# Optimization experiments

Hardware: AMD Instinct MI355X
Metric: run time of the kernel (lower is better)

## Reference

```python
import jax, jax.numpy as jnp
import numpy as np

D_MODEL = 1024
D_STATE = 16
D_CONV = 4
EXPAND = 2
D_INNER = EXPAND * D_MODEL          # 2048
DT_RANK = D_MODEL // 16             # 64 (ceil(d_model/16))
BATCH = 4
SEQ = 2048


def setup_inputs() -> dict:
    key = jax.random.key(0)
    ks = jax.random.split(key, 9)
    s = lambda k, shape, sc: jax.random.normal(k, shape, jnp.float32) * sc
    x = s(ks[0], (BATCH, SEQ, D_MODEL), 1.0)
    W_in = s(ks[1], (2 * D_INNER, D_MODEL), D_MODEL ** -0.5)       # in_proj (no bias)
    conv_w = s(ks[2], (D_INNER, D_CONV), D_CONV ** -0.5)           # depthwise causal conv1d
    conv_b = s(ks[3], (D_INNER,), 0.02)
    W_xproj = s(ks[4], (DT_RANK + 2 * D_STATE, D_INNER), D_INNER ** -0.5)  # x_proj (no bias)
    W_dt = s(ks[5], (D_INNER, DT_RANK), DT_RANK ** -0.5)           # dt_proj weight
    b_dt = jax.random.uniform(ks[6], (D_INNER,), jnp.float32, -4.0, -1.0)  # dt_proj bias (small dt init)
    # S4D-real init: A_log = log([1..d_state]) per channel
    A_log = jnp.log(jnp.tile(jnp.arange(1, D_STATE + 1, dtype=jnp.float32), (D_INNER, 1)))
    D_skip = jnp.ones((D_INNER,), jnp.float32)
    W_out = s(ks[7], (D_MODEL, D_INNER), D_INNER ** -0.5)          # out_proj (no bias)
    return dict(x=x, W_in=W_in, conv_w=conv_w, conv_b=conv_b, W_xproj=W_xproj,
                W_dt=W_dt, b_dt=b_dt, A_log=A_log, D_skip=D_skip, W_out=W_out)


def reference(x, W_in, conv_w, conv_b, W_xproj, W_dt, b_dt, A_log, D_skip, W_out):
    silu = jax.nn.silu
    # in_proj -> split into x stream and gate z
    xz = jnp.einsum('bld,ed->ble', x, W_in)              # (B, L, 2*d_inner)
    xi, z = jnp.split(xz, 2, axis=-1)
    # causal depthwise conv1d (pad left d_conv-1), small fixed K loop
    K = conv_w.shape[1]
    L = xi.shape[1]
    xpad = jnp.pad(xi, ((0, 0), (K - 1, 0), (0, 0)))
    xc = sum(xpad[:, k:k + L, :] * conv_w[:, k] for k in range(K))
    u = silu(xc + conv_b)                                # (B, L, d_inner)
    # x_proj -> dt, B, C
    dbl = jnp.einsum('blc,ec->ble', u, W_xproj)          # (B, L, dt_rank + 2*d_state)
    dt = jax.nn.softplus(jnp.einsum('blr,cr->blc', dbl[..., :DT_RANK], W_dt) + b_dt)  # (B,L,d_inner)
    Bs = dbl[..., DT_RANK:DT_RANK + D_STATE]             # (B, L, d_state)
    Cs = dbl[..., DT_RANK + D_STATE:]                    # (B, L, d_state)
    A = -jnp.exp(A_log)                                  # (d_inner, d_state)

    # selective scan: h_t = exp(dt_t * A) * h_{t-1} + dt_t * B_t * u_t ; y_t = <h_t, C_t>
    def step(h, inp):
        dt_t, B_t, C_t, u_t = inp                        # (B,d_inner),(B,ds),(B,ds),(B,d_inner)
        dA = jnp.exp(dt_t[:, :, None] * A)               # (B, d_inner, d_state)
        h = h * dA + (dt_t * u_t)[:, :, None] * B_t[:, None, :]
        y = jnp.einsum('bcs,bs->bc', h, C_t)
        return h, y

    h0 = jnp.zeros((x.shape[0], D_INNER, D_STATE), x.dtype)
    xs = (jnp.swapaxes(dt, 0, 1), jnp.swapaxes(Bs, 0, 1),
          jnp.swapaxes(Cs, 0, 1), jnp.swapaxes(u, 0, 1))
    _, ys = jax.lax.scan(step, h0, xs)                   # ys: (L, B, d_inner)
    y = jnp.swapaxes(ys, 0, 1) + u * D_skip              # skip connection D*u
    y = y * silu(z)                                      # gate
    return jnp.einsum('blc,dc->bld', y, W_out)           # out_proj -> (B, L, d_model)
```

## Files before the change

### kernel.cpp

```cpp
#include <hip/hip_runtime.h>

#define AS1 __attribute__((address_space(1)))
#define AS3 __attribute__((address_space(3)))

typedef unsigned short ushort_t;
typedef __attribute__((ext_vector_type(8))) short short8;
typedef __attribute__((ext_vector_type(4))) float floatx4;

__device__ __forceinline__ float bf2f(ushort_t h) {
    return __uint_as_float(((unsigned int)h) << 16);
}
__device__ __forceinline__ ushort_t f2bf(float f) {
    unsigned int u = __float_as_uint(f);
    u += 0x7fffu + ((u >> 16) & 1u);
    return (ushort_t)(u >> 16);
}

__global__ __launch_bounds__(256) void cast_all(
    const float* __restrict__ s0, ushort_t* __restrict__ d0,
    const float* __restrict__ s1, ushort_t* __restrict__ d1,
    const float* __restrict__ s2, ushort_t* __restrict__ d2,
    const float* __restrict__ s3, ushort_t* __restrict__ d3,
    const float* __restrict__ s4, ushort_t* __restrict__ d4)
{
    int i = blockIdx.x * 256 + threadIdx.x;
    const float* src; ushort_t* dst; int off;
    if      (i < 2097152) { src = s0; dst = d0; off = i; }
    else if (i < 3145728) { src = s1; dst = d1; off = i - 2097152; }
    else if (i < 3194880) { src = s2; dst = d2; off = i - 3145728; }
    else if (i < 3227648) { src = s3; dst = d3; off = i - 3194880; }
    else                  { src = s4; dst = d4; off = i - 3227648; }
    float4 v = ((const float4*)src)[off];
    ((ushort4*)dst)[off] = make_ushort4(f2bf(v.x), f2bf(v.y), f2bf(v.z), f2bf(v.w));
}

template <int MODE>
__global__ __launch_bounds__(256) void gemm_bt(
    const ushort_t* __restrict__ A, int lda,
    const ushort_t* __restrict__ B, int ldb,
    int K, int Nact, int ldc,
    float* __restrict__ outF, ushort_t* __restrict__ outH,
    ushort_t* __restrict__ outH2, const float* __restrict__ biasF)
{
    constexpr int BM = 128, BN = 128, BK = 64;
    __shared__ ushort_t sA[BM * BK];
    __shared__ ushort_t sB[BN * BK];
    const int tid  = threadIdx.x;
    const int m0   = blockIdx.x * BM;
    const int seg  = (MODE == 4) ? blockIdx.y : 0;
    const int n0   = (MODE == 4) ? 0 : blockIdx.y * BN;
    if (MODE == 4) { A += seg * 512; B += seg * 512; }
    const int lane = tid & 63, wave = tid >> 6;
    const int wm   = (wave & 1) * 64, wn = (wave >> 1) * 64;
    const int lm   = lane & 15, quad = lane >> 4;
    const int lm7  = lane & 7;

    floatx4 acc[4][4];
#pragma unroll
    for (int i = 0; i < 4; ++i)
#pragma unroll
        for (int j = 0; j < 4; ++j)
            acc[i][j] = (floatx4){0.f, 0.f, 0.f, 0.f};

    for (int k0 = 0; k0 < K; k0 += BK) {
        __syncthreads();
#pragma unroll
        for (int r = 0; r < 4; ++r) {
            int g   = r * 256 + tid;
            int row = g >> 3;
            int hh  = (g & 7) ^ (row & 7);
            int col = k0 + hh * 8;
            const ushort_t* gA = A + (size_t)(m0 + row) * lda + col;
            __builtin_amdgcn_global_load_lds((const AS1 void*)gA, (AS3 void*)(&sA[g * 8]), 16, 0, 0);
            int rowB = n0 + row;
            if (rowB >= Nact) rowB = Nact - 1;
            const ushort_t* gB = B + (size_t)rowB * ldb + col;
            __builtin_amdgcn_global_load_lds((const AS1 void*)gB, (AS3 void*)(&sB[g * 8]), 16, 0, 0);
        }
        __syncthreads();

#pragma unroll
        for (int s = 0; s < 2; ++s) {
            short8 af[4], bfr[4];
#pragma unroll
            for (int i = 0; i < 4; ++i) {
                int row = wm + i * 16 + lm;
                int gr  = row * 8 + ((s * 4 + quad) ^ lm7);
                af[i] = *(const short8*)&sA[gr * 8];
            }
#pragma unroll
            for (int j = 0; j < 4; ++j) {
                int row = wn + j * 16 + lm;
                int gr  = row * 8 + ((s * 4 + quad) ^ lm7);
                bfr[j] = *(const short8*)&sB[gr * 8];
            }
#pragma unroll
            for (int i = 0; i < 4; ++i)
#pragma unroll
                for (int j = 0; j < 4; ++j)
                    acc[i][j] = __builtin_amdgcn_mfma_f32_16x16x32_bf16(af[i], bfr[j], acc[i][j], 0, 0, 0);
        }
    }

#pragma unroll
    for (int i = 0; i < 4; ++i) {
#pragma unroll
        for (int j = 0; j < 4; ++j) {
#pragma unroll
            for (int r = 0; r < 4; ++r) {
                int row = m0 + wm + i * 16 + quad * 4 + r;
                int col = n0 + wn + j * 16 + lm;
                float v = acc[i][j][r];
                if (MODE == 0) {
                    if (col < 2048) outH[(size_t)row * 2048 + col] = f2bf(v);
                    else            outH2[(size_t)row * 2048 + (col - 2048)] = f2bf(v);
                } else if (MODE == 2) {
                    float x  = v + biasF[col];
                    float sp = (x > 20.f) ? x : log1pf(__expf(x));
                    _Float16 hv = (_Float16)sp;
                    outH[(size_t)row * ldc + col] = *(ushort_t*)&hv;
                } else if (MODE == 3) {
                    if (col < Nact) outF[(size_t)row * ldc + col] = v;
                } else if (MODE == 4) {
                    if (col < 96)
                        outF[(size_t)seg * 786432 + (size_t)row * 96 + col] = v;
                }
            }
        }
    }
}

__global__ __launch_bounds__(256) void comb3(
    const float* __restrict__ Pg, ushort_t* __restrict__ dbl,
    float* __restrict__ BCf)
{
    int i = blockIdx.x * 256 + threadIdx.x;
    float v = Pg[i] + Pg[i + 786432] + Pg[i + 2 * 786432] + Pg[i + 3 * 786432];
    dbl[i] = f2bf(v);
    int col = i % 96;
    if (col >= 64) BCf[(size_t)(i / 96) * 32 + (col - 64)] = v;
}

__global__ __launch_bounds__(256) void conv_silu_k(
    const ushort_t* __restrict__ xi, const float* __restrict__ conv_w,
    const float* __restrict__ conv_b, ushort_t* __restrict__ u)
{
    int idx = blockIdx.x * 256 + threadIdx.x;
    int c   = idx & 2047;
    int lg  = idx >> 11;
    int b   = lg >> 9;
    int l0  = (lg & 511) * 4;
    const size_t base = ((size_t)b * 2048 + l0) * 2048 + c;

    float w0 = conv_w[c * 4], w1 = conv_w[c * 4 + 1],
          w2 = conv_w[c * 4 + 2], w3 = conv_w[c * 4 + 3];
    float bias = conv_b[c];

    float xv[7];
#pragma unroll
    for (int j = 0; j < 3; ++j)
        xv[j] = (l0 - 3 + j >= 0) ? bf2f(xi[base + (j - 3) * 2048]) : 0.f;
#pragma unroll
    for (int j = 3; j < 7; ++j)
        xv[j] = bf2f(xi[base + (j - 3) * 2048]);

#pragma unroll
    for (int i = 0; i < 4; ++i) {
        float acc = bias + w0 * xv[i] + w1 * xv[i + 1] + w2 * xv[i + 2] + w3 * xv[i + 3];
        float s = acc / (1.f + __expf(-acc));
        u[base + i * 2048] = f2bf(s);
    }
}

constexpr int CH  = 64;
constexpr int NCH = 32;
constexpr int NI  = 4 * 2048 * 16;

__global__ __launch_bounds__(256) void scan_p1(
    const _Float16* __restrict__ dt, const ushort_t* __restrict__ u,
    const float* __restrict__ BC, const float* __restrict__ A_log,
    float* __restrict__ Pbuf, float* __restrict__ Sbuf)
{
    const int tid   = threadIdx.x;
    const int blk   = blockIdx.x;
    const int chunk = blk >> 5;
    const int b     = (blk >> 3) & 3;
    const int c     = ((blk & 7) << 8) + tid;
    const size_t base = (size_t)b * 2048 + chunk * CH;

    float As[16];
#pragma unroll
    for (int s = 0; s < 16; ++s) As[s] = -__expf(A_log[c * 16 + s]);

    float S[16];
#pragma unroll
    for (int s = 0; s < 16; ++s) S[s] = 0.f;
    float cumdt = 0.f;

    for (int t = 0; t < CH; ++t) {
        const size_t r = base + t;
        float dtv = (float)dt[r * 2048 + c];
        float uv  = bf2f(u[r * 2048 + c]);
        float ct  = dtv * uv;
        cumdt += dtv;
#pragma unroll
        for (int s = 0; s < 16; ++s) {
            float a = __expf(dtv * As[s]);
            S[s] = fmaf(S[s], a, ct * BC[r * 32 + s]);
        }
    }
    const size_t ob = (size_t)chunk * NI + (size_t)b * 2048 + c;
#pragma unroll
    for (int s = 0; s < 16; ++s) {
        Pbuf[ob + (size_t)s * 8192] = __expf(As[s] * cumdt);
        Sbuf[ob + (size_t)s * 8192] = S[s];
    }
}

__global__ __launch_bounds__(256) void scan_comb(
    const float* __restrict__ Pbuf, const float* __restrict__ Sbuf,
    float* __restrict__ Hbuf)
{
    const int i = blockIdx.x * 256 + threadIdx.x;
    float hi = 0.f;
#pragma unroll
    for (int k = 0; k < NCH; ++k) {
        Hbuf[(size_t)k * NI + i] = hi;
        hi = Sbuf[(size_t)k * NI + i] + Pbuf[(size_t)k * NI + i] * hi;
    }
}

__global__ __launch_bounds__(256) void scan_p2(
    const _Float16* __restrict__ dt, const ushort_t* __restrict__ u,
    const float* __restrict__ BC, const float* __restrict__ A_log,
    const float* __restrict__ D_skip, const float* __restrict__ Hbuf,
    ushort_t* __restrict__ zy)
{
    const int tid   = threadIdx.x;
    const int blk   = blockIdx.x;
    const int chunk = blk >> 5;
    const int b     = (blk >> 3) & 3;
    const int c     = ((blk & 7) << 8) + tid;
    const size_t base = (size_t)b * 2048 + chunk * CH;

    float As[16], h[16];
#pragma unroll
    for (int s = 0; s < 16; ++s) As[s] = -__expf(A_log[c * 16 + s]);
    const float Dsk = D_skip[c];
    const size_t ob = (size_t)chunk * NI + (size_t)b * 2048 + c;
#pragma unroll
    for (int s = 0; s < 16; ++s) h[s] = Hbuf[ob + (size_t)s * 8192];

    for (int t = 0; t < CH; ++t) {
        const size_t r = base + t;
        float dtv = (float)dt[r * 2048 + c];
        float uv  = bf2f(u[r * 2048 + c]);
        float zv  = bf2f(zy[r * 2048 + c]);
        float ct  = dtv * uv;
        float p0 = 0.f, p1 = 0.f, p2 = 0.f, p3 = 0.f;
#pragma unroll
        for (int s = 0; s < 16; s += 4) {
            float a0 = __expf(dtv * As[s]);
            float a1 = __expf(dtv * As[s + 1]);
            float a2 = __expf(dtv * As[s + 2]);
            float a3 = __expf(dtv * As[s + 3]);
            h[s]     = fmaf(h[s],     a0, ct * BC[r * 32 + s]);
            h[s + 1] = fmaf(h[s + 1], a1, ct * BC[r * 32 + s + 1]);
            h[s + 2] = fmaf(h[s + 2], a2, ct * BC[r * 32 + s + 2]);
            h[s + 3] = fmaf(h[s + 3], a3, ct * BC[r * 32 + s + 3]);
            p0 = fmaf(h[s],     BC[r * 32 + 16 + s],     p0);
            p1 = fmaf(h[s + 1], BC[r * 32 + 16 + s + 1], p1);
            p2 = fmaf(h[s + 2], BC[r * 32 + 16 + s + 2], p2);
            p3 = fmaf(h[s + 3], BC[r * 32 + 16 + s + 3], p3);
        }
        float p = (p0 + p1) + (p2 + p3);
        float g = zv / (1.f + __expf(-zv));
        float yv = (p + uv * Dsk) * g;
        zy[r * 2048 + c] = f2bf(yv);
    }
}

extern "C" void kernel_launch(void* const* d_in, const int* in_sizes, int n_in,
                              void* d_out, int out_size, void* d_ws, size_t ws_size,
                              hipStream_t stream)
{
    const float* x      = (const float*)d_in[0];
    const float* W_in   = (const float*)d_in[1];
    const float* conv_w = (const float*)d_in[2];
    const float* conv_b = (const float*)d_in[3];
    const float* W_xp   = (const float*)d_in[4];
    const float* W_dt   = (const float*)d_in[5];
    const float* b_dt   = (const float*)d_in[6];
    const float* A_log  = (const float*)d_in[7];
    const float* D_skip = (const float*)d_in[8];
    const float* W_out  = (const float*)d_in[9];

    char* ws = (char*)d_ws;
    const size_t MB = 1024 * 1024;
    ushort_t*  xi  = (ushort_t*)(ws);
    ushort_t*  xw  = (ushort_t*)(ws + 32 * MB);
    ushort_t*  Wib = (ushort_t*)(ws + 48 * MB);
    _Float16*  dt  = (_Float16*)(ws);
    float*     Pg  = (float*)(ws + 32 * MB);
    float*     Pb  = (float*)(ws + 32 * MB);
    float*     Sb  = (float*)(ws + 48 * MB);
    ushort_t*  z   = (ushort_t*)(ws + 64 * MB);
    ushort_t*  u   = (ushort_t*)(ws + 96 * MB);
    ushort_t*  dbl = (ushort_t*)(ws + 128 * MB);
    ushort_t*  Wxb = (ushort_t*)(ws + 130 * MB);
    ushort_t*  Wdb = (ushort_t*)(ws + 131 * MB);
    ushort_t*  Wob = (ushort_t*)(ws + 132 * MB);
    float*     BCf = (float*)(ws + 137 * MB);
    float*     Hb  = (float*)(ws + 138 * MB);

    cast_all<<<14656, 256, 0, stream>>>(x, xw, W_in, Wib, W_xp, Wxb, W_dt, Wdb, W_out, Wob);

    gemm_bt<0><<<dim3(64, 32), 256, 0, stream>>>(xw, 1024, Wib, 1024, 1024, 4096, 2048,
                                                 nullptr, xi, z, nullptr);
    conv_silu_k<<<16384, 256, 0, stream>>>(xi, conv_w, conv_b, u);
    gemm_bt<4><<<dim3(64, 4), 256, 0, stream>>>(u, 2048, Wxb, 2048, 512, 96, 96,
                                                Pg, nullptr, nullptr, nullptr);
    comb3<<<3072, 256, 0, stream>>>(Pg, dbl, BCf);
    gemm_bt<2><<<dim3(64, 16), 256, 0, stream>>>(dbl, 96, Wdb, 64, 64, 2048, 2048,
                                                 nullptr, (ushort_t*)dt, nullptr, b_dt);
    scan_p1<<<1024, 256, 0, stream>>>(dt, u, BCf, A_log, Pb, Sb);
    scan_comb<<<512, 256, 0, stream>>>(Pb, Sb, Hb);
    scan_p2<<<1024, 256, 0, stream>>>(dt, u, BCf, A_log, D_skip, Hb, z);
    gemm_bt<3><<<dim3(64, 8), 256, 0, stream>>>(z, 2048, Wob, 2048, 2048, 1024, 1024,
                                                (float*)d_out, nullptr, nullptr, nullptr);
}
```

Measured before the change: 481.2 us.

## Replace in_proj GEMM with 256x256 double-buffered 8-wave pipelined kernel

Adds a new GEMM kernel for the in_proj (8192x4096x1024). It uses 256x256 tiles, 512 threads and double-buffered LDS filled by direct global-to-LDS loads, with XOR-swizzled layout and staged prefetch slots interleaved between MFMA groups. Workgroups are remapped with an XCD-aware swizzle for L2 locality, and s_setprio raises priority around the MFMA blocks. The goal is to hide global load latency and raise MFMA utilization in the largest GEMM, at the cost of 128KB of LDS per block and heavy register pressure.

```diff
diff --git a/kernel.cpp b/kernel.cpp
--- a/kernel.cpp
+++ b/kernel.cpp
@@ -32,6 +32,142 @@
     else                  { src = s4; dst = d4; off = i - 3227648; }
     float4 v = ((const float4*)src)[off];
     ((ushort4*)dst)[off] = make_ushort4(f2bf(v.x), f2bf(v.y), f2bf(v.z), f2bf(v.w));
+}
+
+template <int MODE>
+__global__ __launch_bounds__(512, 2) void gemm8p(
+    const ushort_t* __restrict__ A, int lda,
+    const ushort_t* __restrict__ B, int ldb,
+    int K, ushort_t* __restrict__ outH, ushort_t* __restrict__ outH2,
+    int Mtiles, int Ntiles)
+{
+    __shared__ ushort_t sA[2][16384];
+    __shared__ ushort_t sB[2][16384];
+
+    const int tid = threadIdx.x;
+
+    const int nwg = Mtiles * Ntiles;
+    const int cpx = nwg >> 3;
+    const int flat = blockIdx.x;
+    const int swz = (flat & 7) * cpx + (flat >> 3);
+    const int m0 = (swz % Mtiles) * 256;
+    const int n0 = (swz / Mtiles) * 256;
+
+    const int lane = tid & 63, wave = tid >> 6;
+    const int wm = (wave >> 2) * 128, wn = (wave & 3) * 64;
+    const int lm = lane & 15, quad = lane >> 4, lm7 = lane & 7;
+
+    const int r0 = tid >> 3;
+    const int hh = (tid & 7) ^ (r0 & 7);
+    const ushort_t* pA = A + (size_t)(m0 + r0) * lda + hh * 8;
+    const ushort_t* pB = B + (size_t)(n0 + r0) * ldb + hh * 8;
+
+#define STG_A(buf, tt, rowoff)                                                        \
+    __builtin_amdgcn_global_load_lds(                                                 \
+        (const AS1 void*)(pA + (size_t)(rowoff) * lda + (tt) * 64),                   \
+        (AS3 void*)(&sA[buf][(rowoff) * 64 + tid * 8]), 16, 0, 0)
+#define STG_B(buf, tt, rowoff)                                                        \
+    __builtin_amdgcn_global_load_lds(                                                 \
+        (const AS1 void*)(pB + (size_t)(rowoff) * ldb + (tt) * 64),                   \
+        (AS3 void*)(&sB[buf][(rowoff) * 64 + tid * 8]), 16, 0, 0)
+#define SLOT0(buf, tt) { STG_A(buf, tt, 0);   STG_A(buf, tt, 64);  }
+#define SLOT1(buf, tt) { STG_A(buf, tt, 128); STG_A(buf, tt, 192); }
+#define SLOT2(buf, tt) { STG_B(buf, tt, 0);   STG_B(buf, tt, 64);  }
+#define SLOT3(buf, tt) { STG_B(buf, tt, 128); STG_B(buf, tt, 192); }
+
+#define LD_A(buf, h)                                                                  \
+    { _Pragma("unroll")                                                               \
+      for (int ii = 0; ii < 4; ++ii) {                                                \
+          int row = wm + (h) * 64 + ii * 16 + lm;                                     \
+          a_[ii][0] = *(const short8*)&sA[buf][(row * 8 + (quad ^ lm7)) * 8];         \
+          a_[ii][1] = *(const short8*)&sA[buf][(row * 8 + ((4 + quad) ^ lm7)) * 8];   \
+      } }
+#define LD_B2(buf, j0)                                                                \
+    { _Pragma("unroll")                                                               \
+      for (int jj = 0; jj < 2; ++jj) {                                                \
+          int row = wn + ((j0) + jj) * 16 + lm;                                       \
+          b_[(j0) + jj][0] = *(const short8*)&sB[buf][(row * 8 + (quad ^ lm7)) * 8];  \
+          b_[(j0) + jj][1] = *(const short8*)&sB[buf][(row * 8 + ((4 + quad) ^ lm7)) * 8]; \
+      } }
+#define MFMA16(i0, j0)                                                                \
+    { __builtin_amdgcn_s_setprio(1);                                                  \
+      _Pragma("unroll")                                                               \
+      for (int ii = 0; ii < 4; ++ii) {                                                \
+          _Pragma("unroll")                                                           \
+          for (int jj = 0; jj < 2; ++jj) {                                            \
+              acc[(i0) + ii][(j0) + jj] = __builtin_amdgcn_mfma_f32_16x16x32_bf16(    \
+                  a_[ii][0], b_[(j0) + jj][0], acc[(i0) + ii][(j0) + jj], 0, 0, 0);   \
+              acc[(i0) + ii][(j0) + jj] = __builtin_amdgcn_mfma_f32_16x16x32_bf16(    \
+                  a_[ii][1], b_[(j0) + jj][1], acc[(i0) + ii][(j0) + jj], 0, 0, 0);   \
+          } }                                                                         \
+      __builtin_amdgcn_s_setprio(0); }
+
+    floatx4 acc[8][4];
+#pragma unroll
+    for (int i = 0; i < 8; ++i)
+#pragma unroll
+        for (int j = 0; j < 4; ++j)
+            acc[i][j] = (floatx4){0.f, 0.f, 0.f, 0.f};
+
+    short8 a_[4][2], b_[4][2];
+    const int NT = K >> 6;
+
+    SLOT0(0, 0); SLOT1(0, 0); SLOT2(0, 0); SLOT3(0, 0);
+    SLOT0(1, 1);
+    asm volatile("s_waitcnt vmcnt(2)" ::: "memory");
+    __builtin_amdgcn_s_barrier();
+
+    for (int t = 0; t < NT; ++t) {
+        const int p = t & 1, q = p ^ 1;
+        LD_A(p, 0);
+        LD_B2(p, 0);
+        if (t + 1 < NT) SLOT1(q, t + 1);
+        __builtin_amdgcn_s_barrier();
+        MFMA16(0, 0);
+        __builtin_amdgcn_s_barrier();
+        LD_B2(p, 2);
+        if (t + 1 < NT) SLOT2(q, t + 1);
+        __builtin_amdgcn_s_barrier();
+        MFMA16(0, 2);
+        __builtin_amdgcn_s_barrier();
+        LD_A(p, 1);
+        if (t + 1 < NT) SLOT3(q, t + 1);
+        __builtin_amdgcn_s_barrier();
+        MFMA16(4, 2);
+        __builtin_amdgcn_s_barrier();
+        if (t + 2 < NT) SLOT0(p, t + 2);
+        MFMA16(4, 0);
+        if (t + 2 < NT) { asm volatile("s_waitcnt vmcnt(2)" ::: "memory"); }
+        else            { asm volatile("s_waitcnt vmcnt(0)" ::: "memory"); }
+        __builtin_amdgcn_s_barrier();
+    }
+
+#pragma unroll
+    for (int idx = 0; idx < 8; ++idx) {
+        const int rowb = m0 + wm + (idx >> 2) * 64 + (idx & 3) * 16 + quad * 4;
+#pragma unroll
+        for (int j = 0; j < 4; ++j) {
+            const int col = n0 + wn + j * 16 + lm;
+#pragma unroll
+            for (int r = 0; r < 4; ++r) {
+                float v = acc[idx][j][r];
+                const size_t rr = (size_t)(rowb + r);
+                if (MODE == 0) {
+                    if (col < 2048) outH[rr * 2048 + col] = f2bf(v);
+                    else            outH2[rr * 2048 + (col - 2048)] = f2bf(v);
+                }
+            }
+        }
+    }
+#undef STG_A
+#undef STG_B
+#undef SLOT0
+#undef SLOT1
+#undef SLOT2
+#undef SLOT3
+#undef LD_A
+#undef LD_B2
+#undef MFMA16
 }
 
 template <int MODE>
@@ -111,10 +247,7 @@
                 int row = m0 + wm + i * 16 + quad * 4 + r;
                 int col = n0 + wn + j * 16 + lm;
                 float v = acc[i][j][r];
-                if (MODE == 0) {
-                    if (col < 2048) outH[(size_t)row * 2048 + col] = f2bf(v);
-                    else            outH2[(size_t)row * 2048 + (col - 2048)] = f2bf(v);
-                } else if (MODE == 2) {
+                if (MODE == 2) {
                     float x  = v + biasF[col];
                     float sp = (x > 20.f) ? x : log1pf(__expf(x));
                     _Float16 hv = (_Float16)sp;
@@ -315,8 +448,7 @@
 
     cast_all<<<14656, 256, 0, stream>>>(x, xw, W_in, Wib, W_xp, Wxb, W_dt, Wdb, W_out, Wob);
 
-    gemm_bt<0><<<dim3(64, 32), 256, 0, stream>>>(xw, 1024, Wib, 1024, 1024, 4096, 2048,
-                                                 nullptr, xi, z, nullptr);
+    gemm8p<0><<<512, 512, 0, stream>>>(xw, 1024, Wib, 1024, 1024, xi, z, 32, 16);
     conv_silu_k<<<16384, 256, 0, stream>>>(xi, conv_w, conv_b, u);
     gemm_bt<4><<<dim3(64, 4), 256, 0, stream>>>(u, 2048, Wxb, 2048, 512, 96, 96,
                                                 Pg, nullptr, nullptr, nullptr);
```

Measured after the change: 464.1 us. -3.6%, faster.

## Replace in_proj GEMM with 256x256-tile, 16-wave, double-buffered direct-to-LDS kernel

Applied to the files above, without the earlier changes.

Adds a new gemm16w kernel for the in_proj GEMM. It uses 1024-thread blocks computing 256x256 tiles, with global_load_lds async copies into double-buffered, XOR-swizzled shared memory. Block indices are remapped so that blocks sharing an XCD work on neighbouring tiles, and MFMA issue priority is raised. The goals are better data reuse, overlapping global loads with MFMA work, fewer LDS bank conflicts and better L2 locality. The risks are heavy register and LDS use per block, which lowers occupancy, and a hard-coded grid mapping that only fits this problem shape.

```diff
diff --git a/kernel.cpp b/kernel.cpp
--- a/kernel.cpp
+++ b/kernel.cpp
@@ -32,6 +32,105 @@
     else                  { src = s4; dst = d4; off = i - 3227648; }
     float4 v = ((const float4*)src)[off];
     ((ushort4*)dst)[off] = make_ushort4(f2bf(v.x), f2bf(v.y), f2bf(v.z), f2bf(v.w));
+}
+
+template <int MODE>
+__global__ __launch_bounds__(1024, 4) void gemm16w(
+    const ushort_t* __restrict__ A, int lda,
+    const ushort_t* __restrict__ B, int ldb,
+    int K, ushort_t* __restrict__ outH, ushort_t* __restrict__ outH2)
+{
+    __shared__ ushort_t sA[2][8192];
+    __shared__ ushort_t sB[2][8192];
+
+    const int tid = threadIdx.x;
+
+    const int xcd = blockIdx.x & 7;
+    const int k8  = blockIdx.x >> 3;
+    const int m0  = (((xcd >> 1) << 3) + (k8 >> 3)) * 256;
+    const int n0  = (((xcd & 1) << 3) + (k8 & 7)) * 256;
+
+    const int lane = tid & 63, wave = tid >> 6;
+    const int wm = (wave >> 2) * 64, wn = (wave & 3) * 64;
+    const int lm = lane & 15, quad = lane >> 4;
+    const int lm3 = lane & 3;
+
+    const int r0 = tid >> 2;
+    const int hh = (tid & 3) ^ (r0 & 3);
+    const ushort_t* pA = A + (size_t)(m0 + r0) * lda + hh * 8;
+    const ushort_t* pB = B + (size_t)(n0 + r0) * ldb + hh * 8;
+
+#define STG_A(buf, tt)                                                        \
+    __builtin_amdgcn_global_load_lds((const AS1 void*)(pA + (tt) * 32),       \
+                                     (AS3 void*)(&sA[buf][tid * 8]), 16, 0, 0)
+#define STG_B(buf, tt)                                                        \
+    __builtin_amdgcn_global_load_lds((const AS1 void*)(pB + (tt) * 32),       \
+                                     (AS3 void*)(&sB[buf][tid * 8]), 16, 0, 0)
+#define BARRIER() asm volatile("s_barrier" ::: "memory")
+
+    floatx4 acc[4][4];
+#pragma unroll
+    for (int i = 0; i < 4; ++i)
+#pragma unroll
+        for (int j = 0; j < 4; ++j)
+            acc[i][j] = (floatx4){0.f, 0.f, 0.f, 0.f};
+
+    short8 a_[4], b_[4];
+    const int NT = K >> 5;
+
+    STG_A(0, 0); STG_B(0, 0);
+    STG_A(1, 1); STG_B(1, 1);
+    asm volatile("s_waitcnt vmcnt(2)" ::: "memory");
+    BARRIER();
+
+    for (int t = 0; t < NT; ++t) {
+        const int p = t & 1, q = p ^ 1;
+#pragma unroll
+        for (int i = 0; i < 4; ++i) {
+            int row = wm + i * 16 + lm;
+            a_[i] = *(const short8*)&sA[p][(row * 4 + (quad ^ lm3)) * 8];
+        }
+#pragma unroll
+        for (int j = 0; j < 4; ++j) {
+            int row = wn + j * 16 + lm;
+            b_[j] = *(const short8*)&sB[p][(row * 4 + (quad ^ lm3)) * 8];
+        }
+        if (t + 1 < NT) { STG_A(q, t + 1); STG_B(q, t + 1); }
+        asm volatile("s_waitcnt lgkmcnt(0)" ::: "memory");
+        BARRIER();
+        if (t + 2 < NT) { STG_A(p, t + 2); STG_B(p, t + 2); }
+        __builtin_amdgcn_s_setprio(1);
+#pragma unroll
+        for (int i = 0; i < 4; ++i)
+#pragma unroll
+            for (int j = 0; j < 4; ++j)
+                acc[i][j] = __builtin_amdgcn_mfma_f32_16x16x32_bf16(
+                    a_[i], b_[j], acc[i][j], 0, 0, 0);
+        __builtin_amdgcn_s_setprio(0);
+        if (t + 2 < NT) { asm volatile("s_waitcnt vmcnt(2)" ::: "memory"); }
+        else            { asm volatile("s_waitcnt vmcnt(0)" ::: "memory"); }
+        BARRIER();
+    }
+
+#pragma unroll
+    for (int i = 0; i < 4; ++i) {
+#pragma unroll
+        for (int j = 0; j < 4; ++j) {
+            const int col = n0 + wn + j * 16 + lm;
+#pragma unroll
+            for (int r = 0; r < 4; ++r) {
+                const int row = m0 + wm + i * 16 + quad * 4 + r;
+                float v = acc[i][j][r];
+                if (MODE == 0) {
+                    if (col < 2048) outH[(size_t)row * 2048 + col] = f2bf(v);
+                    else            outH2[(size_t)row * 2048 + (col - 2048)] = f2bf(v);
+                }
+            }
+        }
+    }
+#undef STG_A
+#undef STG_B
+#undef BARRIER
 }
 
 template <int MODE>
@@ -111,10 +210,7 @@
                 int row = m0 + wm + i * 16 + quad * 4 + r;
                 int col = n0 + wn + j * 16 + lm;
                 float v = acc[i][j][r];
-                if (MODE == 0) {
-                    if (col < 2048) outH[(size_t)row * 2048 + col] = f2bf(v);
-                    else            outH2[(size_t)row * 2048 + (col - 2048)] = f2bf(v);
-                } else if (MODE == 2) {
+                if (MODE == 2) {
                     float x  = v + biasF[col];
                     float sp = (x > 20.f) ? x : log1pf(__expf(x));
                     _Float16 hv = (_Float16)sp;
@@ -315,8 +411,7 @@
 
     cast_all<<<14656, 256, 0, stream>>>(x, xw, W_in, Wib, W_xp, Wxb, W_dt, Wdb, W_out, Wob);
 
-    gemm_bt<0><<<dim3(64, 32), 256, 0, stream>>>(xw, 1024, Wib, 1024, 1024, 4096, 2048,
-                                                 nullptr, xi, z, nullptr);
+    gemm16w<0><<<512, 1024, 0, stream>>>(xw, 1024, Wib, 1024, 1024, xi, z);
     conv_silu_k<<<16384, 256, 0, stream>>>(xi, conv_w, conv_b, u);
     gemm_bt<4><<<dim3(64, 4), 256, 0, stream>>>(u, 2048, Wxb, 2048, 512, 96, 96,
                                                 Pg, nullptr, nullptr, nullptr);
```

Measured after the change: 481.1 us. Within noise of the previous version (-0.0%).
